# Kernel tuning notes

Hardware: AMD Instinct MI355X
Metric: run time of the kernel (lower is better)

## Reference

```python
import jax, jax.numpy as jnp
import numpy as np
import itertools

# 3x3x3 neighborhood geometry: 27 cells, offsets in itertools.product order,
# so index 13 is the center voxel.
_POS = np.array(list(itertools.product([-1, 0, 1], repeat=3)))  # [27,3]
_DIFF = _POS[:, None, :] - _POS[None, :, :]
_A18 = (np.abs(_DIFF).sum(-1) <= 2)   # 18-connectivity (scipy structure s in source)
_A26 = (np.abs(_DIFF).max(-1) <= 1)   # 26-connectivity (np.ones((3,3,3)))
_CENTER = 13


def _cc_label_6(fg):
    """Connected-component labels of 3D bool array under 6-connectivity
    (scipy.ndimage.label default structure). Background = 0; each component
    gets a distinct positive id (min linear index + 1) via min-propagation."""
    n = fg.size
    BIG = jnp.int32(n + 2)
    idx = jnp.arange(1, n + 1, dtype=jnp.int32).reshape(fg.shape)
    lab0 = jnp.where(fg, idx, BIG)

    def step(lab):
        p = jnp.pad(lab, 1, mode='constant', constant_values=n + 2)
        m = lab
        m = jnp.minimum(m, p[:-2, 1:-1, 1:-1])
        m = jnp.minimum(m, p[2:, 1:-1, 1:-1])
        m = jnp.minimum(m, p[1:-1, :-2, 1:-1])
        m = jnp.minimum(m, p[1:-1, 2:, 1:-1])
        m = jnp.minimum(m, p[1:-1, 1:-1, :-2])
        m = jnp.minimum(m, p[1:-1, 1:-1, 2:])
        return jnp.where(fg, m, BIG)

    def cond(c):
        return c[1]

    def body(c):
        lab = c[0]
        new = step(lab)
        return (new, jnp.any(new != lab))

    lab, _ = jax.lax.while_loop(cond, body, (lab0, jnp.array(True)))
    return jnp.where(fg, lab, 0)


def _count_components(mask, adj_np):
    """mask: [V,27] bool. Counts connected components of the True cells in each
    27-cell neighborhood under adjacency adj_np (matches scipy label num_features).
    Min-label propagation for 26 steps (>= max path length in a 27-node graph)."""
    BIG = jnp.int32(27)
    ids = jnp.arange(27, dtype=jnp.int32)
    adj = jnp.asarray(adj_np)
    init = jnp.where(mask, ids[None, :], BIG)

    def body(_, lab):
        new = lab
        for j in range(27):
            contrib = jnp.where(mask[:, j], lab[:, j], BIG)[:, None]  # [V,1]
            new = jnp.minimum(new, jnp.where(adj[:, j][None, :], contrib, BIG))
        return jnp.where(mask, new, BIG)

    lab = jax.lax.fori_loop(0, 26, body, init)
    # a component's root keeps its own index -> count roots
    return jnp.sum(mask & (lab == ids[None, :]), axis=1)  # [V]


def _nonsimple_points(x, threshold=0.5):
    """JAX version of label_nonsimple_points: 1.0 where voxel is a non-simple
    point of the thresholded volume, else 0.0."""
    D, H, W = x.shape
    fg = x > threshold
    lab = _cc_label_6(fg)                       # [D,H,W] int32, 0 = background
    p = jnp.pad(lab, 1, mode='edge')            # np.pad(..., 'edge') in source
    nb = jnp.stack(
        [p[dz + 1:dz + 1 + D, dy + 1:dy + 1 + H, dx + 1:dx + 1 + W]
         for dz, dy, dx in _POS], axis=-1).reshape(-1, 27)  # [V,27]
    center = nb[:, _CENTER]
    # Test 1: cells differing from the center's component id (incl. background),
    # 18-connectivity; simple requires exactly one component.
    c1 = _count_components(nb != center[:, None], _A18)
    # Test 2: cells equal to the center's component, center removed,
    # 26-connectivity; simple requires exactly one component.
    m2 = (nb == center[:, None]).at[:, _CENTER].set(False)
    c2 = _count_components(m2, _A26)
    ns = (center != 0) & ((c1 != 1) | (c2 != 1))
    return ns.reshape(x.shape).astype(x.dtype)


def _weight_tensor(x, simple_weight=1.0, non_simple_weight=10.0):
    ns = jax.lax.stop_gradient(_nonsimple_points(x))
    w = simple_weight * (1.0 - ns) + non_simple_weight * ns
    return w * x


def setup_inputs() -> dict:
    key = jax.random.key(0)
    k1, k2 = jax.random.split(key)
    pred = jax.random.normal(k1, (64, 64, 64), dtype=jnp.float32)
    target = jax.random.uniform(k2, (64, 64, 64), dtype=jnp.float32)
    return {"pred": pred, "target": target}


def reference(pred, target):
    wp = _weight_tensor(pred)
    wl = _weight_tensor(target)
    # err = -(wl * -log(1+e^{-wp}) + (1-wl) * -log(1+e^{wp}))
    err = wl * jax.nn.softplus(-wp) + (1.0 - wl) * jax.nn.softplus(wp)
    return jnp.sum(err)
```

## Files before the change

kernel.cpp:

```cpp
#include <hip/hip_runtime.h>

#define NINV 0xFFFFFFFFu
static constexpr int D = 64, H = 64, W = 64;
static constexpr int NVOX = D * H * W;
static constexpr int NTOT = 2 * NVOX;


__device__ __forceinline__ unsigned find_c(unsigned* P, unsigned i) {
    unsigned p = P[i];
    while (p != i) {
        unsigned gp = P[p];
        if (gp == p) return p;
        P[i] = gp;
        i = gp;
        p = P[i];
    }
    return i;
}

__device__ void unite(unsigned* P, unsigned a, unsigned b) {
    for (;;) {
        a = find_c(P, a);
        b = find_c(P, b);
        if (a == b) return;
        if (a > b) { unsigned t = a; a = b; b = t; }
        unsigned old = atomicCAS(&P[b], b, a);
        if (old == b || old == a) return;
        b = old;
    }
}


__global__ __launch_bounds__(512) void local_ccl_k(const float* __restrict__ pred,
                                                   const float* __restrict__ target,
                                                   unsigned* __restrict__ parent) {
    __shared__ unsigned lab[512];
    int tb  = blockIdx.x & 511;
    int vol = blockIdx.x >> 9;
    const float* src = vol ? target : pred;
    int tx = (tb & 7) << 3;
    int ty = ((tb >> 3) & 7) << 3;
    int tz = (tb >> 6) << 3;

    int l = threadIdx.x;
    int lx = l & 7, ly = (l >> 3) & 7, lz = l >> 6;
    int g = ((tz + lz) << 12) + ((ty + ly) << 6) + (tx + lx);

    bool fg = src[g] > 0.5f;
    lab[l] = fg ? (unsigned)l : NINV;
    __syncthreads();

    for (;;) {
        int my_changed = 0;
        if (fg) {
            unsigned cur = lab[l];
            unsigned m = cur;
            if (lx > 0) m = min(m, lab[l - 1]);
            if (lx < 7) m = min(m, lab[l + 1]);
            if (ly > 0) m = min(m, lab[l - 8]);
            if (ly < 7) m = min(m, lab[l + 8]);
            if (lz > 0) m = min(m, lab[l - 64]);
            if (lz < 7) m = min(m, lab[l + 64]);
            for (;;) { unsigned p = lab[m]; if (p >= m) break; m = p; }
            if (m < cur) { lab[l] = m; my_changed = 1; }
        }
        if (__syncthreads_count(my_changed) == 0) break;
    }

    unsigned r = NINV;
    if (fg) {
        unsigned rr = lab[l];
        r = (unsigned)(vol * NVOX)
          + (unsigned)(((tz + (int)(rr >> 6)) << 12)
                     + ((ty + (int)((rr >> 3) & 7)) << 6)
                     +  (tx + (int)(rr & 7)));
    }
    parent[vol * NVOX + g] = r;
}


static constexpr int FACE_PER_DIR = 7 * 64 * 64;
static constexpr int FACE_PER_VOL = 3 * FACE_PER_DIR;
static constexpr int FACE_TOT     = 2 * FACE_PER_VOL;

__global__ void merge_k(unsigned* __restrict__ parent) {
    int t = blockIdx.x * blockDim.x + threadIdx.x;
    if (t >= FACE_TOT) return;
    int vol = t / FACE_PER_VOL;
    int r   = t - vol * FACE_PER_VOL;
    int dir = r / FACE_PER_DIR;
    int s   = r - dir * FACE_PER_DIR;
    int plane = s >> 12;
    int q     = s & 4095;
    int x, y, z, stride;
    if (dir == 0)      { x = plane * 8 + 7; y = q & 63; z = q >> 6; stride = 1; }
    else if (dir == 1) { y = plane * 8 + 7; x = q & 63; z = q >> 6; stride = 64; }
    else               { z = plane * 8 + 7; x = q & 63; y = q >> 6; stride = 4096; }
    int i = vol * NVOX + (z << 12) + (y << 6) + x;
    if (parent[i] == NINV || parent[i + stride] == NINV) return;
    unite(parent, (unsigned)i, (unsigned)(i + stride));
}


__global__ void flatten_k(unsigned* __restrict__ parent) {
    int i = blockIdx.x * blockDim.x + threadIdx.x;
    if (i >= NTOT) return;
    unsigned p = parent[i];
    if (p == NINV) return;
    unsigned r = p, q;
    while ((q = parent[r]) != r) r = q;
    parent[i] = r;
}


__device__ __forceinline__ int count_components(unsigned mask, const unsigned* adj) {
    int count = 0;
    while (mask) {
        unsigned comp = mask & (0u - mask);
        for (;;) {
            unsigned acc = comp;
            unsigned t = comp;
            while (t) {
                int b = __ffs(t) - 1;
                acc |= adj[b];
                t &= t - 1;
            }
            acc &= mask;
            if (acc == comp) break;
            comp = acc;
        }
        mask &= ~comp;
        ++count;
    }
    return count;
}

__device__ __forceinline__ float weight_for(int i, int x, int y, int z,
                                            const unsigned* __restrict__ lab,
                                            const unsigned* sA18, const unsigned* sA26) {
    unsigned c = lab[i];
    if (c == NINV) return 1.0f;
    unsigned same = 0;
    int k = 0;
    #pragma unroll
    for (int dz = -1; dz <= 1; ++dz) {
        int zz = z + dz; zz = zz < 0 ? 0 : (zz > D - 1 ? D - 1 : zz);
        #pragma unroll
        for (int dy = -1; dy <= 1; ++dy) {
            int yy = y + dy; yy = yy < 0 ? 0 : (yy > H - 1 ? H - 1 : yy);
            int base = (zz << 12) + (yy << 6);
            #pragma unroll
            for (int dx = -1; dx <= 1; ++dx) {
                int xx = x + dx; xx = xx < 0 ? 0 : (xx > W - 1 ? W - 1 : xx);
                same |= (lab[base + xx] == c ? 1u : 0u) << k;
                ++k;
            }
        }
    }
    unsigned mask1 = (~same) & 0x07FFFFFFu;
    unsigned mask2 = same & ~(1u << 13);
    int c1 = count_components(mask1, sA18);
    int c2 = count_components(mask2, sA26);
    return ((c1 != 1) || (c2 != 1)) ? 10.0f : 1.0f;
}

__global__ void final_k(const float* __restrict__ pred, const float* __restrict__ target,
                        const unsigned* __restrict__ labP, const unsigned* __restrict__ labT,
                        float* __restrict__ out) {
    __shared__ unsigned sA18[27], sA26[27];
    if (threadIdx.x < 27) {
        int ii = threadIdx.x;
        int iz = ii / 9, iy = (ii / 3) % 3, ix = ii % 3;
        unsigned m18 = 0, m26 = 0;
        for (int j = 0; j < 27; ++j) {
            int jz = j / 9, jy = (j / 3) % 3, jx = j % 3;
            int az = iz - jz; az = az < 0 ? -az : az;
            int ay = iy - jy; ay = ay < 0 ? -ay : ay;
            int ax = ix - jx; ax = ax < 0 ? -ax : ax;
            if (az + ay + ax <= 2) m18 |= 1u << j;
            if (az <= 1 && ay <= 1 && ax <= 1) m26 |= 1u << j;
        }
        sA18[ii] = m18; sA26[ii] = m26;
    }
    __syncthreads();

    int i = blockIdx.x * blockDim.x + threadIdx.x;
    float err = 0.0f;
    if (i < NVOX) {
        int x = i & (W - 1);
        int y = (i >> 6) & (H - 1);
        int z = i >> 12;
        float wP = weight_for(i, x, y, z, labP, sA18, sA26);
        float wT = weight_for(i, x, y, z, labT, sA18, sA26);
        float wp = wP * pred[i];
        float wl = wT * target[i];
        float l1pe = log1pf(expf(-fabsf(wp)));
        float sp_pos = fmaxf(wp, 0.0f) + l1pe;
        float sp_neg = fmaxf(-wp, 0.0f) + l1pe;
        err = wl * sp_neg + (1.0f - wl) * sp_pos;
    }

    #pragma unroll
    for (int o = 32; o > 0; o >>= 1) err += __shfl_down(err, o, 64);
    __shared__ float sred[4];
    int lane = threadIdx.x & 63;
    int wv = threadIdx.x >> 6;
    if (lane == 0) sred[wv] = err;
    __syncthreads();
    if (threadIdx.x == 0) {
        atomicAdd(out, sred[0] + sred[1] + sred[2] + sred[3]);
    }
}


extern "C" void kernel_launch(void* const* d_in, const int* in_sizes, int n_in,
                              void* d_out, int out_size, void* d_ws, size_t ws_size,
                              hipStream_t stream) {
    const float* pred   = (const float*)d_in[0];
    const float* target = (const float*)d_in[1];
    float* out = (float*)d_out;
    unsigned* parent = (unsigned*)d_ws;

    hipMemsetAsync(d_out, 0, sizeof(float), stream);

    local_ccl_k<<<1024, 512, 0, stream>>>(pred, target, parent);
    merge_k<<<(FACE_TOT + 255) / 256, 256, 0, stream>>>(parent);
    flatten_k<<<NTOT / 256, 256, 0, stream>>>(parent);
    final_k<<<NVOX / 256, 256, 0, stream>>>(pred, target,
                                            parent, parent + NVOX, out);
}
```

Measured before the change: 130.9 us.

## Dedupe boundary unions per wave and tile final stencil through LDS halo

The merge kernel now assigns one wave to each 8x8 tile face and deduplicates identical (root, root) pairs across lanes with shuffles, so only one lane per distinct pair calls unite, cutting redundant atomics and contention. The final kernel now processes 8x8x8 tiles with a 10x10x10 halo of labels staged in shared memory for both volumes, replacing 27 clamped global loads per voxel with LDS reads. The costs are a 64-iteration shuffle loop per merge lane and extra LDS use that may lower occupancy in the final kernel.

```diff
diff --git a/kernel.cpp b/kernel.cpp
--- a/kernel.cpp
+++ b/kernel.cpp
@@ -79,26 +79,40 @@
 }
 
 
-static constexpr int FACE_PER_DIR = 7 * 64 * 64;
-static constexpr int FACE_PER_VOL = 3 * FACE_PER_DIR;
-static constexpr int FACE_TOT     = 2 * FACE_PER_VOL;
+static constexpr int FACES_PER_DIR = 7 * 8 * 8;
+static constexpr int FACES_PER_VOL = 3 * FACES_PER_DIR;
+static constexpr int FACES_TOT     = 2 * FACES_PER_VOL;
 
 __global__ void merge_k(unsigned* __restrict__ parent) {
-    int t = blockIdx.x * blockDim.x + threadIdx.x;
-    if (t >= FACE_TOT) return;
-    int vol = t / FACE_PER_VOL;
-    int r   = t - vol * FACE_PER_VOL;
-    int dir = r / FACE_PER_DIR;
-    int s   = r - dir * FACE_PER_DIR;
-    int plane = s >> 12;
-    int q     = s & 4095;
+    int wave = (int)((blockIdx.x * blockDim.x + threadIdx.x) >> 6);
+    int lane = threadIdx.x & 63;
+    if (wave >= FACES_TOT) return;
+    int vol = wave / FACES_PER_VOL;
+    int f   = wave - vol * FACES_PER_VOL;
+    int dir = f / FACES_PER_DIR;
+    int ff  = f - dir * FACES_PER_DIR;
+    int plane = ff >> 6;
+    int tf    = ff & 63;
+    int a0 = ((tf & 7) << 3) + (lane & 7);
+    int a1 = ((tf >> 3) << 3) + (lane >> 3);
     int x, y, z, stride;
-    if (dir == 0)      { x = plane * 8 + 7; y = q & 63; z = q >> 6; stride = 1; }
-    else if (dir == 1) { y = plane * 8 + 7; x = q & 63; z = q >> 6; stride = 64; }
-    else               { z = plane * 8 + 7; x = q & 63; y = q >> 6; stride = 4096; }
+    if (dir == 0)      { x = plane * 8 + 7; y = a0; z = a1; stride = 1; }
+    else if (dir == 1) { y = plane * 8 + 7; x = a0; z = a1; stride = 64; }
+    else               { z = plane * 8 + 7; x = a0; y = a1; stride = 4096; }
     int i = vol * NVOX + (z << 12) + (y << 6) + x;
-    if (parent[i] == NINV || parent[i + stride] == NINV) return;
-    unite(parent, (unsigned)i, (unsigned)(i + stride));
+
+    unsigned ra = parent[i];
+    unsigned rb = parent[i + stride];
+    bool valid = (ra != NINV) && (rb != NINV);
+    unsigned long long key = valid ? (((unsigned long long)ra << 32) | rb) : ~0ull;
+
+    bool leader = valid;
+    #pragma unroll 8
+    for (int j = 0; j < 64; ++j) {
+        unsigned long long kj = __shfl(key, j, 64);
+        if (j < lane && kj == key) leader = false;
+    }
+    if (leader) unite(parent, ra, rb);
 }
 
 
@@ -135,24 +149,22 @@
     return count;
 }
 
-__device__ __forceinline__ float weight_for(int i, int x, int y, int z,
-                                            const unsigned* __restrict__ lab,
+__device__ __forceinline__ float weight_lds(const unsigned* __restrict__ h,
+                                            int lx, int ly, int lz,
                                             const unsigned* sA18, const unsigned* sA26) {
-    unsigned c = lab[i];
+    int ctr = (lz + 1) * 100 + (ly + 1) * 10 + (lx + 1);
+    unsigned c = h[ctr];
     if (c == NINV) return 1.0f;
     unsigned same = 0;
     int k = 0;
     #pragma unroll
-    for (int dz = -1; dz <= 1; ++dz) {
-        int zz = z + dz; zz = zz < 0 ? 0 : (zz > D - 1 ? D - 1 : zz);
+    for (int dz = 0; dz <= 2; ++dz) {
         #pragma unroll
-        for (int dy = -1; dy <= 1; ++dy) {
-            int yy = y + dy; yy = yy < 0 ? 0 : (yy > H - 1 ? H - 1 : yy);
-            int base = (zz << 12) + (yy << 6);
+        for (int dy = 0; dy <= 2; ++dy) {
+            int base = (lz + dz) * 100 + (ly + dy) * 10 + lx;
             #pragma unroll
-            for (int dx = -1; dx <= 1; ++dx) {
-                int xx = x + dx; xx = xx < 0 ? 0 : (xx > W - 1 ? W - 1 : xx);
-                same |= (lab[base + xx] == c ? 1u : 0u) << k;
+            for (int dx = 0; dx <= 2; ++dx) {
+                same |= (h[base + dx] == c ? 1u : 0u) << k;
                 ++k;
             }
         }
@@ -164,13 +176,18 @@
     return ((c1 != 1) || (c2 != 1)) ? 10.0f : 1.0f;
 }
 
-__global__ void final_k(const float* __restrict__ pred, const float* __restrict__ target,
-                        const unsigned* __restrict__ labP, const unsigned* __restrict__ labT,
-                        float* __restrict__ out) {
+__global__ __launch_bounds__(512) void final_k(const float* __restrict__ pred,
+                                               const float* __restrict__ target,
+                                               const unsigned* __restrict__ labP,
+                                               const unsigned* __restrict__ labT,
+                                               float* __restrict__ out) {
     __shared__ unsigned sA18[27], sA26[27];
-    if (threadIdx.x < 27) {
-        int ii = threadIdx.x;
-        int iz = ii / 9, iy = (ii / 3) % 3, ix = ii % 3;
+    __shared__ unsigned hP[1000], hT[1000];
+    __shared__ float sred[8];
+
+    int l = threadIdx.x;
+    if (l < 27) {
+        int iz = l / 9, iy = (l / 3) % 3, ix = l % 3;
         unsigned m18 = 0, m26 = 0;
         for (int j = 0; j < 27; ++j) {
             int jz = j / 9, jy = (j / 3) % 3, jx = j % 3;
@@ -180,35 +197,48 @@
             if (az + ay + ax <= 2) m18 |= 1u << j;
             if (az <= 1 && ay <= 1 && ax <= 1) m26 |= 1u << j;
         }
-        sA18[ii] = m18; sA26[ii] = m26;
+        sA18[l] = m18; sA26[l] = m26;
+    }
+
+    int tb = blockIdx.x;
+    int tx = (tb & 7) << 3;
+    int ty = ((tb >> 3) & 7) << 3;
+    int tz = (tb >> 6) << 3;
+
+    for (int e = l; e < 1000; e += 512) {
+        int hx = e % 10, hy = (e / 10) % 10, hz = e / 100;
+        int gx = min(max(tx + hx - 1, 0), 63);
+        int gy = min(max(ty + hy - 1, 0), 63);
+        int gz = min(max(tz + hz - 1, 0), 63);
+        int g = (gz << 12) + (gy << 6) + gx;
+        hP[e] = labP[g];
+        hT[e] = labT[g];
     }
     __syncthreads();
 
-    int i = blockIdx.x * blockDim.x + threadIdx.x;
-    float err = 0.0f;
-    if (i < NVOX) {
-        int x = i & (W - 1);
-        int y = (i >> 6) & (H - 1);
-        int z = i >> 12;
-        float wP = weight_for(i, x, y, z, labP, sA18, sA26);
-        float wT = weight_for(i, x, y, z, labT, sA18, sA26);
-        float wp = wP * pred[i];
-        float wl = wT * target[i];
-        float l1pe = log1pf(expf(-fabsf(wp)));
-        float sp_pos = fmaxf(wp, 0.0f) + l1pe;
-        float sp_neg = fmaxf(-wp, 0.0f) + l1pe;
-        err = wl * sp_neg + (1.0f - wl) * sp_pos;
-    }
+    int lx = l & 7, ly = (l >> 3) & 7, lz = l >> 6;
+    int g = ((tz + lz) << 12) + ((ty + ly) << 6) + (tx + lx);
+
+    float wP = weight_lds(hP, lx, ly, lz, sA18, sA26);
+    float wT = weight_lds(hT, lx, ly, lz, sA18, sA26);
+    float wp = wP * pred[g];
+    float wl = wT * target[g];
+    float l1pe = log1pf(expf(-fabsf(wp)));
+    float sp_pos = fmaxf(wp, 0.0f) + l1pe;
+    float sp_neg = fmaxf(-wp, 0.0f) + l1pe;
+    float err = wl * sp_neg + (1.0f - wl) * sp_pos;
 
     #pragma unroll
     for (int o = 32; o > 0; o >>= 1) err += __shfl_down(err, o, 64);
-    __shared__ float sred[4];
-    int lane = threadIdx.x & 63;
-    int wv = threadIdx.x >> 6;
+    int lane = l & 63;
+    int wv = l >> 6;
     if (lane == 0) sred[wv] = err;
     __syncthreads();
-    if (threadIdx.x == 0) {
-        atomicAdd(out, sred[0] + sred[1] + sred[2] + sred[3]);
+    if (l == 0) {
+        float s = 0.0f;
+        #pragma unroll
+        for (int w = 0; w < 8; ++w) s += sred[w];
+        atomicAdd(out, s);
     }
 }
 
@@ -224,8 +254,7 @@
     hipMemsetAsync(d_out, 0, sizeof(float), stream);
 
     local_ccl_k<<<1024, 512, 0, stream>>>(pred, target, parent);
-    merge_k<<<(FACE_TOT + 255) / 256, 256, 0, stream>>>(parent);
+    merge_k<<<FACES_TOT * 64 / 256, 256, 0, stream>>>(parent);
     flatten_k<<<NTOT / 256, 256, 0, stream>>>(parent);
-    final_k<<<NVOX / 256, 256, 0, stream>>>(pred, target,
-                                            parent, parent + NVOX, out);
-}
+    final_k<<<512, 512, 0, stream>>>(pred, target, parent, parent + NVOX, out);
+}
```

Measured after the change: 124.6 us. 4.8% less time.
